# Kernel tuning notes

Measured on AMD Instinct MI355X. Metric: run time of the kernel, lower is better.

Reference implementation:

```python
import jax, jax.numpy as jnp
import numpy as np

N_NODES = 100000
N_EDGES = 1600000
IN_FEATS = 256
OUT_FEATS = 128
GAMMA = 1.0


def setup_inputs() -> dict:
    key = jax.random.key(0)
    k1, k2, k3, k4, k5 = jax.random.split(key, 5)
    glorot = np.sqrt(6.0 / (IN_FEATS + OUT_FEATS)).astype(np.float32)
    feat = jax.random.normal(k1, (N_NODES, IN_FEATS), dtype=jnp.float32)
    W_mean = jax.random.uniform(k2, (IN_FEATS, OUT_FEATS), dtype=jnp.float32, minval=-glorot, maxval=glorot)
    W_var = jax.random.uniform(k3, (IN_FEATS, OUT_FEATS), dtype=jnp.float32, minval=-glorot, maxval=glorot)
    src = jax.random.randint(k4, (N_EDGES,), 0, N_NODES, dtype=jnp.int64 if jax.config.jax_enable_x64 else jnp.int32)
    dst = jax.random.randint(k5, (N_EDGES,), 0, N_NODES, dtype=jnp.int64 if jax.config.jax_enable_x64 else jnp.int32)
    return {"feat": feat, "W_mean": W_mean, "W_var": W_var, "src": src, "dst": dst}


def reference(feat, W_mean, W_var, src, dst):
    # dense projections + relu (no bias, as bias=False)
    mean = jax.nn.relu(jnp.matmul(feat, W_mean))   # [N, F]
    var = jax.nn.relu(jnp.matmul(feat, W_var))     # [N, F]
    attention = jnp.exp(-GAMMA * var)
    # in-degrees from dst edge endpoints, clamped to >= 1
    degs = jax.ops.segment_sum(jnp.ones_like(dst, dtype=jnp.float32), dst, num_segments=N_NODES)
    degs = jnp.clip(degs, 1.0)
    norm1 = (degs ** -0.5)[:, None]                # [N, 1] = D^{-1/2}
    norm2 = norm1 * norm1                          # [N, 1] = D^{-1}
    m_msg = mean * attention * norm1
    v_msg = var * attention * attention * norm2
    # copy_src + sum aggregation (SpMM over edge list)
    mean_agg = jax.ops.segment_sum(m_msg[src], dst, num_segments=N_NODES) * norm1
    var_agg = jax.ops.segment_sum(v_msg[src], dst, num_segments=N_NODES) * norm2
    return mean_agg, var_agg
```

## Files before the change

### kernel.cpp

```cpp
#include <hip/hip_runtime.h>
#include <hip/hip_bf16.h>

#define N_NODES 100000
#define N_EDGES 1600000
#define OUTF 128
#define INF 256
#define SCAN_CHUNK 1024
#define SCAN_BLOCKS 98
#define M_TILES 6250

typedef _Float16 f16;
typedef _Float16 half8 __attribute__((ext_vector_type(8)));
typedef _Float16 half4 __attribute__((ext_vector_type(4)));
typedef _Float16 half2v __attribute__((ext_vector_type(2)));
typedef float floatx4 __attribute__((ext_vector_type(4)));

__global__ void count_rank_kernel(const int* __restrict__ dst, int E,
                                  int* __restrict__ deg, int* __restrict__ rank) {
    int i = blockIdx.x * blockDim.x + threadIdx.x;
    if (i < E) rank[i] = atomicAdd(&deg[dst[i]], 1);
}

__global__ __launch_bounds__(256) void scan_partial_kernel(const int* __restrict__ deg, int n,
                                                           int* __restrict__ partial) {
    __shared__ int red[256];
    int b = blockIdx.x, t = threadIdx.x;
    int base = b * SCAN_CHUNK;
    int s = 0;
    for (int i = t; i < SCAN_CHUNK; i += 256) {
        int idx = base + i;
        if (idx < n) s += deg[idx];
    }
    red[t] = s;
    __syncthreads();
    for (int off = 128; off > 0; off >>= 1) {
        if (t < off) red[t] += red[t + off];
        __syncthreads();
    }
    if (t == 0) partial[b] = red[0];
}

__global__ __launch_bounds__(128) void scan_top_kernel(int* __restrict__ partial, int nb,
                                                       int* __restrict__ row_start, int n) {
    __shared__ int sc[128];
    int t = threadIdx.x;
    int v = (t < nb) ? partial[t] : 0;
    sc[t] = v;
    __syncthreads();
    for (int off = 1; off < 128; off <<= 1) {
        int val = sc[t];
        int add = (t >= off) ? sc[t - off] : 0;
        __syncthreads();
        sc[t] = val + add;
        __syncthreads();
    }
    if (t < nb) partial[t] = sc[t] - v;
    if (t == 127) row_start[n] = sc[127];
}

__global__ __launch_bounds__(256) void scan_final_kernel(const int* __restrict__ deg, int n,
                                                         const int* __restrict__ partial,
                                                         int* __restrict__ row_start,
                                                         float* __restrict__ norm1,
                                                         float* __restrict__ norm2) {
    __shared__ int sc[256];
    int b = blockIdx.x, t = threadIdx.x;
    int base = b * SCAN_CHUNK + t * 4;
    int v[4];
    int tsum = 0;
#pragma unroll
    for (int j = 0; j < 4; j++) {
        int idx = base + j;
        v[j] = (idx < n) ? deg[idx] : 0;
        tsum += v[j];
    }
    sc[t] = tsum;
    __syncthreads();
    for (int off = 1; off < 256; off <<= 1) {
        int val = sc[t];
        int add = (t >= off) ? sc[t - off] : 0;
        __syncthreads();
        sc[t] = val + add;
        __syncthreads();
    }
    int run = sc[t] - tsum + partial[b];
#pragma unroll
    for (int j = 0; j < 4; j++) {
        int idx = base + j;
        if (idx < n) {
            row_start[idx] = run;
            float d = (float)(v[j] > 0 ? v[j] : 1);
            norm1[idx] = rsqrtf(d);
            norm2[idx] = 1.0f / d;
            run += v[j];
        }
    }
}

__global__ void scatter_edges_kernel(const int* __restrict__ src, const int* __restrict__ dst,
                                     const int* __restrict__ rank,
                                     const int* __restrict__ row_start,
                                     int E, int* __restrict__ srcs_sorted) {
    int i = blockIdx.x * blockDim.x + threadIdx.x;
    if (i < E) {
        srcs_sorted[row_start[dst[i]] + rank[i]] = src[i];
    }
}

__global__ __launch_bounds__(256) void convert_B_kernel(const float* __restrict__ Wm,
                                                        const float* __restrict__ Wv,
                                                        f16* __restrict__ Bt) {
    int k = threadIdx.x;
    int ng = blockIdx.x;
    int g = ng >> 4, i = ng & 15;
    int ch = g >> 3, w = (g >> 1) & 3, cg = g & 1;
    int col = ch * 64 + w * 16 + i;
    const float* srcW = cg ? Wv : Wm;
    Bt[ng * 256 + k] = (f16)srcW[k * 128 + col];
}

__global__ __launch_bounds__(256, 3) void proj_mfma_kernel(const float* __restrict__ feat,
                                                           const f16* __restrict__ Bt,
                                                           const float* __restrict__ norm1,
                                                           const float* __restrict__ norm2,
                                                           f16* __restrict__ msg) {
    __shared__ float As[2][16 * 256];

    int tid = threadIdx.x;
    int w = tid >> 6;
    int lane = tid & 63;
    int quad = lane >> 4;
    int l15 = lane & 15;
    int ch = blockIdx.x & 1;
    int tbase = blockIdx.x >> 1;

    half8 b[2][8];
#pragma unroll
    for (int cg = 0; cg < 2; cg++) {
        int g = ch * 8 + w * 2 + cg;
        const f16* bp = Bt + (size_t)(g * 16 + l15) * 256 + quad * 8;
#pragma unroll
        for (int kf = 0; kf < 8; kf++) {
            b[cg][kf] = *(const half8*)(bp + kf * 32);
        }
    }
#pragma unroll
    for (int cg = 0; cg < 2; cg++) {
#pragma unroll
        for (int kf = 0; kf < 8; kf++) {
            asm volatile("" : "+v"(b[cg][kf]));
        }
    }

    int col = ch * 64 + w * 16 + l15;

    int swz = (l15 & 7) << 4;
    int rb0 = l15 * 1024 + ((quad * 32) ^ swz);
    int rb1 = l15 * 1024 + ((quad * 32 + 16) ^ swz);

    int lsw = lane * 16;

    auto stage = [&](int buf, int t) {
        int m0 = t * 16;
#pragma unroll
        for (int j = 0; j < 4; j++) {
            int r = w * 4 + j;
            const char* gp = (const char*)(feat + (size_t)(m0 + r) * 256)
                             + (lsw ^ ((r & 7) << 4));
            char* lp = (char*)&As[buf][0] + r * 1024;
            __builtin_amdgcn_global_load_lds(
                (const __attribute__((address_space(1))) void*)gp,
                (__attribute__((address_space(3))) void*)lp, 16, 0, 0);
        }
    };

    stage(0, tbase);
    int cur = 0;

    for (int t = tbase; t < M_TILES; t += 1250) {
        __syncthreads();

        int tn = t + 1250;
        if (tn < M_TILES) stage(cur ^ 1, tn);

        const char* ab = (const char*)&As[cur][0];
        half8 a[8];
#pragma unroll
        for (int kf = 0; kf < 8; kf++) {
            floatx4 f0 = *(const floatx4*)(ab + rb0 + kf * 128);
            floatx4 f1 = *(const floatx4*)(ab + rb1 + kf * 128);
            half8 h;
            h[0] = (f16)f0.x; h[1] = (f16)f0.y; h[2] = (f16)f0.z; h[3] = (f16)f0.w;
            h[4] = (f16)f1.x; h[5] = (f16)f1.y; h[6] = (f16)f1.z; h[7] = (f16)f1.w;
            a[kf] = h;
        }

        int m0 = t * 16;
        float s1r[4], s2r[4];
#pragma unroll
        for (int r = 0; r < 4; r++) {
            int node = m0 + quad * 4 + r;
            s1r[r] = norm1[node];
            s2r[r] = norm2[node];
        }

        floatx4 acc0 = (floatx4){0.f, 0.f, 0.f, 0.f};
        floatx4 acc1 = (floatx4){0.f, 0.f, 0.f, 0.f};
#pragma unroll
        for (int kf = 0; kf < 8; kf++) {
            acc0 = __builtin_amdgcn_mfma_f32_16x16x32_f16(a[kf], b[0][kf], acc0, 0, 0, 0);
            acc1 = __builtin_amdgcn_mfma_f32_16x16x32_f16(a[kf], b[1][kf], acc1, 0, 0, 0);
        }

#pragma unroll
        for (int r = 0; r < 4; r++) {
            int node = m0 + quad * 4 + r;
            float m = fmaxf(acc0[r], 0.f);
            float v = fmaxf(acc1[r], 0.f);
            float att = __expf(-v);
            half2v pr;
            pr[0] = (f16)(m * att * s1r[r]);
            pr[1] = (f16)(v * att * att * s2r[r]);
            *(half2v*)(msg + (size_t)node * 256 + col * 2) = pr;
        }
        cur ^= 1;
    }
}

__global__ __launch_bounds__(256) void agg_kernel(const int* __restrict__ row_start,
                                                  const int* __restrict__ srcs,
                                                  const f16* __restrict__ msg,
                                                  const float* __restrict__ norm1,
                                                  const float* __restrict__ norm2,
                                                  float* __restrict__ out_mean,
                                                  float* __restrict__ out_var) {
    int d = blockIdx.x * 4 + (threadIdx.x >> 6);
    int lane = threadIdx.x & 63;
    int s0 = row_start[d];
    int s1 = row_start[d + 1];
    float am0 = 0.f, am1 = 0.f, av0 = 0.f, av1 = 0.f;
    int i = s0;
    for (; i + 7 < s1; i += 8) {
        half4 h[8];
#pragma unroll
        for (int j = 0; j < 8; j++) {
            h[j] = *(const half4*)(msg + (size_t)srcs[i + j] * 256 + lane * 4);
        }
#pragma unroll
        for (int j = 0; j < 8; j++) {
            am0 += (float)h[j][0];
            av0 += (float)h[j][1];
            am1 += (float)h[j][2];
            av1 += (float)h[j][3];
        }
    }
    for (; i < s1; i++) {
        half4 ha = *(const half4*)(msg + (size_t)srcs[i] * 256 + lane * 4);
        am0 += (float)ha[0];
        av0 += (float)ha[1];
        am1 += (float)ha[2];
        av1 += (float)ha[3];
    }
    float k1 = norm1[d], k2 = norm2[d];
    float2 om = make_float2(am0 * k1, am1 * k1);
    float2 ov = make_float2(av0 * k2, av1 * k2);
    *(float2*)(out_mean + (size_t)d * 128 + lane * 2) = om;
    *(float2*)(out_var + (size_t)d * 128 + lane * 2) = ov;
}

extern "C" void kernel_launch(void* const* d_in, const int* in_sizes, int n_in,
                              void* d_out, int out_size, void* d_ws, size_t ws_size,
                              hipStream_t stream) {
    const float* feat = (const float*)d_in[0];
    const float* Wm = (const float*)d_in[1];
    const float* Wv = (const float*)d_in[2];
    const int* src = (const int*)d_in[3];
    const int* dst = (const int*)d_in[4];
    float* out = (float*)d_out;

    const int N = N_NODES;
    const int E = N_EDGES;

    char* wsp = (char*)d_ws;
    auto carve = [&](size_t bytes) {
        char* p = wsp;
        wsp += (bytes + 255) & ~(size_t)255;
        return p;
    };
    f16* msg = (f16*)carve((size_t)N * 256 * sizeof(f16));
    f16* Bt = (f16*)carve((size_t)256 * 256 * sizeof(f16));
    int* srcs_sorted = (int*)carve((size_t)E * 4);
    int* rank = (int*)carve((size_t)E * 4);
    int* deg = (int*)carve((size_t)N * 4);
    int* row_start = (int*)carve((size_t)(N + 1) * 4);
    float* norm1 = (float*)carve((size_t)N * 4);
    float* norm2 = (float*)carve((size_t)N * 4);
    int* partial = (int*)carve(128 * 4);

    hipMemsetAsync(deg, 0, (size_t)N * 4, stream);

    count_rank_kernel<<<(E + 255) / 256, 256, 0, stream>>>(dst, E, deg, rank);
    convert_B_kernel<<<256, 256, 0, stream>>>(Wm, Wv, Bt);
    scan_partial_kernel<<<SCAN_BLOCKS, 256, 0, stream>>>(deg, N, partial);
    scan_top_kernel<<<1, 128, 0, stream>>>(partial, SCAN_BLOCKS, row_start, N);
    scan_final_kernel<<<SCAN_BLOCKS, 256, 0, stream>>>(deg, N, partial, row_start, norm1, norm2);
    scatter_edges_kernel<<<(E + 255) / 256, 256, 0, stream>>>(src, dst, rank, row_start, E,
                                                              srcs_sorted);
    proj_mfma_kernel<<<2500, 256, 0, stream>>>(feat, Bt, norm1, norm2, msg);
    agg_kernel<<<N / 4, 256, 0, stream>>>(row_start, srcs_sorted, msg, norm1, norm2,
                                          out, out + (size_t)N * OUTF);
}
```

Measured before the change: 434.9 us.

## Widen aggregation gathers to half8 with split-wave edges and remap projection blocks

The aggregation kernel now splits each wave into two halves. Each half handles alternate edges and loads 16-byte half8 vectors instead of 8-byte half4, and the halves are combined with a cross-half shuffle. Output is written with 16-byte nontemporal stores from one half. The projection kernel also remaps block indices so that blocks sharing a column half are grouped in runs of eight tiles, which may improve cache locality for the B operand and the feature rows. The intent is fewer, wider memory transactions per gathered row and more edges in flight, at the cost of one shuffle reduction and idle lanes during the store.

```diff
diff --git a/kernel.cpp b/kernel.cpp
--- a/kernel.cpp
+++ b/kernel.cpp
@@ -131,8 +131,18 @@
     int lane = tid & 63;
     int quad = lane >> 4;
     int l15 = lane & 15;
-    int ch = blockIdx.x & 1;
-    int tbase = blockIdx.x >> 1;
+
+    int bidx = blockIdx.x;
+    int jj, ch;
+    if (bidx < 2496) {
+        jj = (bidx >> 4) * 8 + (bidx & 7);
+        ch = (bidx >> 3) & 1;
+    } else {
+        int r = bidx - 2496;
+        jj = 1248 + (r >> 1);
+        ch = r & 1;
+    }
+    int tbase = jj;
 
     half8 b[2][8];
 #pragma unroll
@@ -236,36 +246,60 @@
                                                   float* __restrict__ out_var) {
     int d = blockIdx.x * 4 + (threadIdx.x >> 6);
     int lane = threadIdx.x & 63;
+    int half = lane >> 5;
+    int j = lane & 31;
+
     int s0 = row_start[d];
     int s1 = row_start[d + 1];
-    float am0 = 0.f, am1 = 0.f, av0 = 0.f, av1 = 0.f;
-    int i = s0;
-    for (; i + 7 < s1; i += 8) {
-        half4 h[8];
-#pragma unroll
-        for (int j = 0; j < 8; j++) {
-            h[j] = *(const half4*)(msg + (size_t)srcs[i + j] * 256 + lane * 4);
-        }
-#pragma unroll
-        for (int j = 0; j < 8; j++) {
-            am0 += (float)h[j][0];
-            av0 += (float)h[j][1];
-            am1 += (float)h[j][2];
-            av1 += (float)h[j][3];
-        }
-    }
-    for (; i < s1; i++) {
-        half4 ha = *(const half4*)(msg + (size_t)srcs[i] * 256 + lane * 4);
+
+    float am0 = 0.f, am1 = 0.f, am2 = 0.f, am3 = 0.f;
+    float av0 = 0.f, av1 = 0.f, av2 = 0.f, av3 = 0.f;
+
+    int i = s0 + half;
+    for (; i + 6 < s1; i += 8) {
+        int sa = srcs[i], sb = srcs[i + 2], sc = srcs[i + 4], sd = srcs[i + 6];
+        half8 ha = *(const half8*)(msg + (size_t)sa * 256 + j * 8);
+        half8 hb = *(const half8*)(msg + (size_t)sb * 256 + j * 8);
+        half8 hc = *(const half8*)(msg + (size_t)sc * 256 + j * 8);
+        half8 hd = *(const half8*)(msg + (size_t)sd * 256 + j * 8);
+        am0 += (float)ha[0] + (float)hb[0] + (float)hc[0] + (float)hd[0];
+        av0 += (float)ha[1] + (float)hb[1] + (float)hc[1] + (float)hd[1];
+        am1 += (float)ha[2] + (float)hb[2] + (float)hc[2] + (float)hd[2];
+        av1 += (float)ha[3] + (float)hb[3] + (float)hc[3] + (float)hd[3];
+        am2 += (float)ha[4] + (float)hb[4] + (float)hc[4] + (float)hd[4];
+        av2 += (float)ha[5] + (float)hb[5] + (float)hc[5] + (float)hd[5];
+        am3 += (float)ha[6] + (float)hb[6] + (float)hc[6] + (float)hd[6];
+        av3 += (float)ha[7] + (float)hb[7] + (float)hc[7] + (float)hd[7];
+    }
+    for (; i < s1; i += 2) {
+        int sa = srcs[i];
+        half8 ha = *(const half8*)(msg + (size_t)sa * 256 + j * 8);
         am0 += (float)ha[0];
         av0 += (float)ha[1];
         am1 += (float)ha[2];
         av1 += (float)ha[3];
-    }
-    float k1 = norm1[d], k2 = norm2[d];
-    float2 om = make_float2(am0 * k1, am1 * k1);
-    float2 ov = make_float2(av0 * k2, av1 * k2);
-    *(float2*)(out_mean + (size_t)d * 128 + lane * 2) = om;
-    *(float2*)(out_var + (size_t)d * 128 + lane * 2) = ov;
+        am2 += (float)ha[4];
+        av2 += (float)ha[5];
+        am3 += (float)ha[6];
+        av3 += (float)ha[7];
+    }
+
+    am0 += __shfl_xor(am0, 32, 64);
+    am1 += __shfl_xor(am1, 32, 64);
+    am2 += __shfl_xor(am2, 32, 64);
+    am3 += __shfl_xor(am3, 32, 64);
+    av0 += __shfl_xor(av0, 32, 64);
+    av1 += __shfl_xor(av1, 32, 64);
+    av2 += __shfl_xor(av2, 32, 64);
+    av3 += __shfl_xor(av3, 32, 64);
+
+    if (half == 0) {
+        float k1 = norm1[d], k2 = norm2[d];
+        floatx4 om = {am0 * k1, am1 * k1, am2 * k1, am3 * k1};
+        floatx4 ov = {av0 * k2, av1 * k2, av2 * k2, av3 * k2};
+        __builtin_nontemporal_store(om, (floatx4*)(out_mean + (size_t)d * 128 + j * 4));
+        __builtin_nontemporal_store(ov, (floatx4*)(out_var + (size_t)d * 128 + j * 4));
+    }
 }
 
 extern "C" void kernel_launch(void* const* d_in, const int* in_sizes, int n_in,
```

After: 430.1 us. Within noise of the previous version (-1.1%).
